# Optimization experiments

Hardware: AMD Instinct MI355X
Metric: run time of the kernel (lower is better)

Reference implementation:

```python
import jax, jax.numpy as jnp
import numpy as np

N = 64      # num_agents
Z = 512     # z_dim
D = 512     # d_model


def setup_inputs() -> dict:
    key = jax.random.key(0)
    k0, k1, k2, k3, k4 = jax.random.split(key, 5)
    z = jax.random.normal(k0, (N, Z), dtype=jnp.float32)
    # per-agent unshared projections (bias=False), kaiming-uniform-ish scale
    s = 1.0 / np.sqrt(Z).astype(np.float32)
    Wq = jax.random.normal(k1, (N, D, Z), dtype=jnp.float32) * s
    Wk = jax.random.normal(k2, (N, D, Z), dtype=jnp.float32) * s
    Wv = jax.random.normal(k3, (N, D, Z), dtype=jnp.float32) * s
    Wi = jax.random.normal(k4, (Z, D), dtype=jnp.float32) * (1.0 / np.sqrt(D).astype(np.float32))
    bi = jnp.zeros((Z,), dtype=jnp.float32)
    return {"z": z, "Wq": Wq, "Wk": Wk, "Wv": Wv, "Wi": Wi, "bi": bi}


def reference(z, Wq, Wk, Wv, Wi, bi):
    n, d = z.shape[0], Wq.shape[1]
    scale = jnp.sqrt(jnp.asarray(d, z.dtype))
    # batched per-agent GEMV: Q[n] = Wq[n] @ z[n]
    Q = jnp.einsum('ndz,nz->nd', Wq, z)
    K = jnp.einsum('ndz,nz->nd', Wk, z)
    V = jnp.einsum('ndz,nz->nd', Wv, z)
    # S[i, j] = <K_i, Q_j> / sqrt(d); complete graph minus self-edges
    S = (K @ Q.T) / scale
    S = jnp.where(jnp.eye(n, dtype=bool), -jnp.inf, S)
    alpha = jax.nn.softmax(S, axis=0)            # softmax over senders i for each receiver j
    messages = jnp.einsum('ij,id->jd', alpha, V)  # (N, D)
    # infer aux loss: each sender i is inferred identically by all N-1 receivers,
    # so the mean over N*(N-1) pairs equals the mean over i of per-agent MSE.
    hat = V @ Wi.T + bi                           # (N, Z)
    per_agent_mse = jnp.mean((hat - z) ** 2, axis=1)
    total_infer_loss = jnp.mean(per_agent_mse)
    return messages, total_infer_loss
```

## Files before the change

### kernel.cpp

```cpp
#include <hip/hip_runtime.h>
#include <math.h>

#define NAG 64
#define ZD  512
#define DM  512

struct GBuf {
    float4 w0, w1, w2, w3, w4, w5, w6, w7;
    float4 zA, zB;
    float* outp;
};

__device__ __forceinline__ void issue_group(
    int rowBase, int lane,
    const float* __restrict__ z,
    const float* __restrict__ Wq, const float* __restrict__ Wk,
    const float* __restrict__ Wv,
    float* __restrict__ Q, float* __restrict__ K, float* __restrict__ V,
    GBuf& b)
{
    const int m   = rowBase >> 15;
    const int rem = rowBase & 32767;
    const int n   = rem >> 9;
    const int d0  = rem & 511;
    const float* __restrict__ W = (m == 0) ? Wq : ((m == 1) ? Wk : Wv);
    float* __restrict__ O       = (m == 0) ? Q  : ((m == 1) ? K  : V);

    const float* zr = z + n * ZD;
    b.zA = *reinterpret_cast<const float4*>(zr + lane * 4);
    b.zB = *reinterpret_cast<const float4*>(zr + 256 + lane * 4);

    const float* Wb = W + ((size_t)(n * DM + d0)) * ZD;
    b.w0 = *reinterpret_cast<const float4*>(Wb + lane * 4);
    b.w1 = *reinterpret_cast<const float4*>(Wb + 256 + lane * 4);
    b.w2 = *reinterpret_cast<const float4*>(Wb + ZD + lane * 4);
    b.w3 = *reinterpret_cast<const float4*>(Wb + ZD + 256 + lane * 4);
    b.w4 = *reinterpret_cast<const float4*>(Wb + 2 * ZD + lane * 4);
    b.w5 = *reinterpret_cast<const float4*>(Wb + 2 * ZD + 256 + lane * 4);
    b.w6 = *reinterpret_cast<const float4*>(Wb + 3 * ZD + lane * 4);
    b.w7 = *reinterpret_cast<const float4*>(Wb + 3 * ZD + 256 + lane * 4);
    b.outp = O + n * DM + d0;
}

__device__ __forceinline__ void compute_group(int lane, const GBuf& b)
{
    float a0 = b.w0.x*b.zA.x + b.w0.y*b.zA.y + b.w0.z*b.zA.z + b.w0.w*b.zA.w
             + b.w1.x*b.zB.x + b.w1.y*b.zB.y + b.w1.z*b.zB.z + b.w1.w*b.zB.w;
    float a1 = b.w2.x*b.zA.x + b.w2.y*b.zA.y + b.w2.z*b.zA.z + b.w2.w*b.zA.w
             + b.w3.x*b.zB.x + b.w3.y*b.zB.y + b.w3.z*b.zB.z + b.w3.w*b.zB.w;
    float a2 = b.w4.x*b.zA.x + b.w4.y*b.zA.y + b.w4.z*b.zA.z + b.w4.w*b.zA.w
             + b.w5.x*b.zB.x + b.w5.y*b.zB.y + b.w5.z*b.zB.z + b.w5.w*b.zB.w;
    float a3 = b.w6.x*b.zA.x + b.w6.y*b.zA.y + b.w6.z*b.zA.z + b.w6.w*b.zA.w
             + b.w7.x*b.zB.x + b.w7.y*b.zB.y + b.w7.z*b.zB.z + b.w7.w*b.zB.w;
#pragma unroll
    for (int off = 32; off > 0; off >>= 1) {
        a0 += __shfl_down(a0, off);
        a1 += __shfl_down(a1, off);
        a2 += __shfl_down(a2, off);
        a3 += __shfl_down(a3, off);
    }
    if (lane == 0) {
        b.outp[0] = a0; b.outp[1] = a1; b.outp[2] = a2; b.outp[3] = a3;
    }
}

__global__ __launch_bounds__(256) void qkv_gemv_kernel(
    const float* __restrict__ z,
    const float* __restrict__ Wq,
    const float* __restrict__ Wk,
    const float* __restrict__ Wv,
    float* __restrict__ Q, float* __restrict__ K, float* __restrict__ V)
{
    const int wave = threadIdx.x >> 6;
    const int lane = threadIdx.x & 63;
    const int gw = blockIdx.x * 4 + wave;
    const int rb = gw * 12;

    GBuf A, B;
    issue_group(rb,     lane, z, Wq, Wk, Wv, Q, K, V, A);
    issue_group(rb + 4, lane, z, Wq, Wk, Wv, Q, K, V, B);
    compute_group(lane, A);
    issue_group(rb + 8, lane, z, Wq, Wk, Wv, Q, K, V, A);
    compute_group(lane, B);
    compute_group(lane, A);
}

__global__ __launch_bounds__(256) void attn_infer_kernel(
    const float* __restrict__ Q, const float* __restrict__ K,
    const float* __restrict__ V, const float* __restrict__ Wi,
    const float* __restrict__ bi, const float* __restrict__ z,
    float* __restrict__ out, float* __restrict__ zp_partial)
{
    __shared__ __align__(16) float sbuf[DM];
    __shared__ float Sc[NAG];
    __shared__ float Al[NAG];
    const int t = threadIdx.x;

    if (blockIdx.x < NAG) {
        const int j = blockIdx.x;
        sbuf[t]       = Q[j * DM + t];
        sbuf[t + 256] = Q[j * DM + t + 256];
        __syncthreads();

        const int i = t >> 2;
        const int c = t & 3;
        const float* Krow = K + i * DM + c * 128;
        const float* Qsub = sbuf + c * 128;
        float p = 0.f;
#pragma unroll
        for (int k = 0; k < 32; ++k) {
            float4 kv = *reinterpret_cast<const float4*>(Krow + k * 4);
            float4 qv = *reinterpret_cast<const float4*>(Qsub + k * 4);
            p += kv.x*qv.x + kv.y*qv.y + kv.z*qv.z + kv.w*qv.w;
        }
        p += __shfl_xor(p, 1);
        p += __shfl_xor(p, 2);
        if (c == 0)
            Sc[i] = (i == j) ? -INFINITY : p * 0.044194173824159216f;
        __syncthreads();

        if (t < 64) {
            float s = Sc[t];
            float mx = s;
#pragma unroll
            for (int off = 32; off > 0; off >>= 1) mx = fmaxf(mx, __shfl_xor(mx, off));
            float e = expf(s - mx);
            float sum = e;
#pragma unroll
            for (int off = 32; off > 0; off >>= 1) sum += __shfl_xor(sum, off);
            Al[t] = e / sum;
        }
        __syncthreads();

#pragma unroll
        for (int dd = 0; dd < 2; ++dd) {
            const int d = t + dd * 256;
            float acc = 0.f;
            for (int i2 = 0; i2 < NAG; ++i2) acc += Al[i2] * V[i2 * DM + d];
            out[j * DM + d] = acc;
        }
    } else {
        const int zp = blockIdx.x - NAG;
        const float* wr = Wi + (size_t)zp * DM;
        sbuf[t]       = wr[t];
        sbuf[t + 256] = wr[t + 256];
        __syncthreads();

        const int i = t >> 2;
        const int c = t & 3;
        const float* Vrow = V + i * DM + c * 128;
        const float* Wsub = sbuf + c * 128;
        float p = 0.f;
#pragma unroll
        for (int k = 0; k < 32; ++k) {
            float4 vv = *reinterpret_cast<const float4*>(Vrow + k * 4);
            float4 wv = *reinterpret_cast<const float4*>(Wsub + k * 4);
            p += vv.x*wv.x + vv.y*wv.y + vv.z*wv.z + vv.w*wv.w;
        }
        p += __shfl_xor(p, 1);
        p += __shfl_xor(p, 2);

        float e2 = 0.f;
        if (c == 0) {
            float e = p + bi[zp] - z[i * ZD + zp];
            e2 = e * e;
        }
#pragma unroll
        for (int off = 32; off > 0; off >>= 1) e2 += __shfl_down(e2, off);

        const int wv2 = t >> 6;
        const int ln  = t & 63;
        if (ln == 0) Sc[wv2] = e2;
        __syncthreads();
        if (t == 0) zp_partial[zp] = Sc[0] + Sc[1] + Sc[2] + Sc[3];
    }
}

__global__ __launch_bounds__(64) void loss_reduce_kernel(
    const float* __restrict__ zp_partial, float* __restrict__ out)
{
    float v = 0.f;
#pragma unroll
    for (int k = 0; k < 8; ++k) v += zp_partial[threadIdx.x + k * 64];
#pragma unroll
    for (int off = 32; off > 0; off >>= 1) v += __shfl_down(v, off);
    if (threadIdx.x == 0) out[NAG * DM] = v * (1.0f / (NAG * ZD));
}

extern "C" void kernel_launch(void* const* d_in, const int* in_sizes, int n_in,
                              void* d_out, int out_size, void* d_ws, size_t ws_size,
                              hipStream_t stream) {
    const float* z  = (const float*)d_in[0];
    const float* Wq = (const float*)d_in[1];
    const float* Wk = (const float*)d_in[2];
    const float* Wv = (const float*)d_in[3];
    const float* Wi = (const float*)d_in[4];
    const float* bi = (const float*)d_in[5];
    float* out = (float*)d_out;

    float* Q = (float*)d_ws;
    float* K = Q + NAG * DM;
    float* V = K + NAG * DM;
    float* partial = V + NAG * DM;

    hipLaunchKernelGGL(qkv_gemv_kernel, dim3(2048), dim3(256), 0, stream,
                       z, Wq, Wk, Wv, Q, K, V);
    hipLaunchKernelGGL(attn_infer_kernel, dim3(NAG + ZD), dim3(256), 0, stream,
                       Q, K, V, Wi, bi, z, out, partial);
    hipLaunchKernelGGL(loss_reduce_kernel, dim3(1), dim3(64), 0, stream,
                       partial, out);
}
```

Measured before the change: 52.28 us.

## Stage QKV weights through LDS with async global_load_lds double buffering

Rewrites the batched QKV GEMV so each 128-thread block stages 128 weight rows in 64-column tiles into LDS using direct global-to-LDS loads, double-buffered across the K dimension. Each thread then computes one full output row, which removes the cross-lane shuffle reductions, and a rotated slot swizzle avoids LDS bank conflicts. The aim is deeper memory-level parallelism on a bandwidth-bound 200 MB weight stream. In exchange the grid shrinks to 768 small blocks and a barrier is added per tile, which may lower occupancy and in-flight bytes.

```diff
diff --git a/kernel.cpp b/kernel.cpp
--- a/kernel.cpp
+++ b/kernel.cpp
@@ -4,85 +4,96 @@
 #define NAG 64
 #define ZD  512
 #define DM  512
-
-struct GBuf {
-    float4 w0, w1, w2, w3, w4, w5, w6, w7;
-    float4 zA, zB;
-    float* outp;
-};
-
-__device__ __forceinline__ void issue_group(
-    int rowBase, int lane,
-    const float* __restrict__ z,
-    const float* __restrict__ Wq, const float* __restrict__ Wk,
-    const float* __restrict__ Wv,
-    float* __restrict__ Q, float* __restrict__ K, float* __restrict__ V,
-    GBuf& b)
-{
-    const int m   = rowBase >> 15;
-    const int rem = rowBase & 32767;
-    const int n   = rem >> 9;
-    const int d0  = rem & 511;
-    const float* __restrict__ W = (m == 0) ? Wq : ((m == 1) ? Wk : Wv);
-    float* __restrict__ O       = (m == 0) ? Q  : ((m == 1) ? K  : V);
-
-    const float* zr = z + n * ZD;
-    b.zA = *reinterpret_cast<const float4*>(zr + lane * 4);
-    b.zB = *reinterpret_cast<const float4*>(zr + 256 + lane * 4);
-
-    const float* Wb = W + ((size_t)(n * DM + d0)) * ZD;
-    b.w0 = *reinterpret_cast<const float4*>(Wb + lane * 4);
-    b.w1 = *reinterpret_cast<const float4*>(Wb + 256 + lane * 4);
-    b.w2 = *reinterpret_cast<const float4*>(Wb + ZD + lane * 4);
-    b.w3 = *reinterpret_cast<const float4*>(Wb + ZD + 256 + lane * 4);
-    b.w4 = *reinterpret_cast<const float4*>(Wb + 2 * ZD + lane * 4);
-    b.w5 = *reinterpret_cast<const float4*>(Wb + 2 * ZD + 256 + lane * 4);
-    b.w6 = *reinterpret_cast<const float4*>(Wb + 3 * ZD + lane * 4);
-    b.w7 = *reinterpret_cast<const float4*>(Wb + 3 * ZD + 256 + lane * 4);
-    b.outp = O + n * DM + d0;
-}
-
-__device__ __forceinline__ void compute_group(int lane, const GBuf& b)
-{
-    float a0 = b.w0.x*b.zA.x + b.w0.y*b.zA.y + b.w0.z*b.zA.z + b.w0.w*b.zA.w
-             + b.w1.x*b.zB.x + b.w1.y*b.zB.y + b.w1.z*b.zB.z + b.w1.w*b.zB.w;
-    float a1 = b.w2.x*b.zA.x + b.w2.y*b.zA.y + b.w2.z*b.zA.z + b.w2.w*b.zA.w
-             + b.w3.x*b.zB.x + b.w3.y*b.zB.y + b.w3.z*b.zB.z + b.w3.w*b.zB.w;
-    float a2 = b.w4.x*b.zA.x + b.w4.y*b.zA.y + b.w4.z*b.zA.z + b.w4.w*b.zA.w
-             + b.w5.x*b.zB.x + b.w5.y*b.zB.y + b.w5.z*b.zB.z + b.w5.w*b.zB.w;
-    float a3 = b.w6.x*b.zA.x + b.w6.y*b.zA.y + b.w6.z*b.zA.z + b.w6.w*b.zA.w
-             + b.w7.x*b.zB.x + b.w7.y*b.zB.y + b.w7.z*b.zB.z + b.w7.w*b.zB.w;
-#pragma unroll
-    for (int off = 32; off > 0; off >>= 1) {
-        a0 += __shfl_down(a0, off);
-        a1 += __shfl_down(a1, off);
-        a2 += __shfl_down(a2, off);
-        a3 += __shfl_down(a3, off);
-    }
-    if (lane == 0) {
-        b.outp[0] = a0; b.outp[1] = a1; b.outp[2] = a2; b.outp[3] = a3;
-    }
-}
-
-__global__ __launch_bounds__(256) void qkv_gemv_kernel(
+#define KT  64
+#define NT  (ZD / KT)
+#define RPB 128
+
+__device__ __forceinline__ void gload_lds16(const float* g, float* l)
+{
+    __builtin_amdgcn_global_load_lds(
+        (const __attribute__((address_space(1))) unsigned int*)g,
+        (__attribute__((address_space(3))) unsigned int*)l,
+        16, 0, 0);
+}
+
+__global__ __launch_bounds__(128) void qkv_gemv_kernel(
     const float* __restrict__ z,
     const float* __restrict__ Wq,
     const float* __restrict__ Wk,
     const float* __restrict__ Wv,
     float* __restrict__ Q, float* __restrict__ K, float* __restrict__ V)
 {
-    const int wave = threadIdx.x >> 6;
-    const int lane = threadIdx.x & 63;
-    const int gw = blockIdx.x * 4 + wave;
-    const int rb = gw * 12;
-
-    GBuf A, B;
-    issue_group(rb,     lane, z, Wq, Wk, Wv, Q, K, V, A);
-    issue_group(rb + 4, lane, z, Wq, Wk, Wv, Q, K, V, B);
-    compute_group(lane, A);
-    issue_group(rb + 8, lane, z, Wq, Wk, Wv, Q, K, V, A);
-    compute_group(lane, B);
-    compute_group(lane, A);
+    __shared__ __align__(16) float Wt[2][RPB * KT];
+
+    const int tid  = threadIdx.x;
+    const int wv   = tid >> 6;
+    const int lane = tid & 63;
+
+    const int R0 = blockIdx.x * RPB;
+    const int m  = R0 >> 15;
+    const int n  = (R0 >> 9) & 63;
+    const int d0 = R0 & 511;
+
+    const float* __restrict__ Wm = ((m == 0) ? Wq : (m == 1) ? Wk : Wv)
+                                   + ((size_t)(n * DM + d0)) * ZD;
+    float* __restrict__ O        = ((m == 0) ? Q : (m == 1) ? K : V)
+                                   + n * DM + d0;
+    const float* __restrict__ zn = z + n * ZD;
+
+    const int srow  = wv * 64 + (lane >> 4);
+    const int sslot = lane & 15;
+
+#pragma unroll
+    for (int i = 0; i < 16; ++i) {
+        const int row   = srow + i * 4;
+        const int gslot = (sslot - row) & 15;
+        gload_lds16(Wm + (size_t)row * ZD + gslot * 4,
+                    &Wt[0][(wv * 64 + i * 4) * KT]);
+    }
+    __syncthreads();
+
+    const int r = tid;
+    float a0 = 0.f, a1 = 0.f, a2 = 0.f, a3 = 0.f;
+    int buf = 0;
+
+#pragma unroll
+    for (int t = 0; t < NT; ++t) {
+        if (t + 1 < NT) {
+            const int k0n = (t + 1) * KT;
+#pragma unroll
+            for (int i = 0; i < 16; ++i) {
+                const int row   = srow + i * 4;
+                const int gslot = (sslot - row) & 15;
+                gload_lds16(Wm + (size_t)row * ZD + k0n + gslot * 4,
+                            &Wt[buf ^ 1][(wv * 64 + i * 4) * KT]);
+            }
+        }
+        const int k0 = t * KT;
+        const float* wrow = &Wt[buf][r * KT];
+#pragma unroll
+        for (int j = 0; j < 16; j += 4) {
+            const int s0 = (j + 0 + r) & 15;
+            const int s1 = (j + 1 + r) & 15;
+            const int s2 = (j + 2 + r) & 15;
+            const int s3 = (j + 3 + r) & 15;
+            const float4 w0 = *reinterpret_cast<const float4*>(wrow + s0 * 4);
+            const float4 w1 = *reinterpret_cast<const float4*>(wrow + s1 * 4);
+            const float4 w2 = *reinterpret_cast<const float4*>(wrow + s2 * 4);
+            const float4 w3 = *reinterpret_cast<const float4*>(wrow + s3 * 4);
+            const float4 z0 = *reinterpret_cast<const float4*>(zn + k0 + (j + 0) * 4);
+            const float4 z1 = *reinterpret_cast<const float4*>(zn + k0 + (j + 1) * 4);
+            const float4 z2 = *reinterpret_cast<const float4*>(zn + k0 + (j + 2) * 4);
+            const float4 z3 = *reinterpret_cast<const float4*>(zn + k0 + (j + 3) * 4);
+            a0 += w0.x*z0.x + w0.y*z0.y + w0.z*z0.z + w0.w*z0.w;
+            a1 += w1.x*z1.x + w1.y*z1.y + w1.z*z1.z + w1.w*z1.w;
+            a2 += w2.x*z2.x + w2.y*z2.y + w2.z*z2.z + w2.w*z2.w;
+            a3 += w3.x*z3.x + w3.y*z3.y + w3.z*z3.z + w3.w*z3.w;
+        }
+        __syncthreads();
+        buf ^= 1;
+    }
+
+    O[r] = a0 + a1 + a2 + a3;
 }
 
 __global__ __launch_bounds__(256) void attn_infer_kernel(
@@ -203,7 +214,7 @@
     float* V = K + NAG * DM;
     float* partial = V + NAG * DM;
 
-    hipLaunchKernelGGL(qkv_gemv_kernel, dim3(2048), dim3(256), 0, stream,
+    hipLaunchKernelGGL(qkv_gemv_kernel, dim3(768), dim3(128), 0, stream,
                        z, Wq, Wk, Wv, Q, K, V);
     hipLaunchKernelGGL(attn_infer_kernel, dim3(NAG + ZD), dim3(256), 0, stream,
                        Q, K, V, Wi, bi, z, out, partial);
```

After: 62.85 us. 20.2% more time.
